# Kernel optimization log

Hardware: AMD Instinct MI355X
Metric: run time of the kernel (lower is better)

The kernel has to match this reference:

```python
import jax, jax.numpy as jnp
import numpy as np
from jax import lax

# SLAYER neuron / simulation constants (from netParams)
THETA = 10.0       # spike threshold
TAU_SR = 10.0      # synaptic (PSP) time constant
TAU_REF = 1.0      # refractory time constant
SCALE_REF = 2.0    # refractory scale
TAU_RHO = 1.0      # surrogate-gradient width (unused in fwd)
K_PSP = 32         # truncation length of SRM alpha kernel
K_REF = 16         # truncation length of refractory kernel

_t = np.arange(K_PSP, dtype=np.float64)
PSP_KERN = jnp.asarray((_t / TAU_SR) * np.exp(1.0 - _t / TAU_SR), jnp.float32)  # [K_PSP]
_tr = np.arange(1, K_REF + 1, dtype=np.float64)
REF_KERN = jnp.asarray(-SCALE_REF * THETA * (_tr / TAU_REF) * np.exp(1.0 - _tr / TAU_REF), jnp.float32)  # [K_REF]


def psp(x):
    """Causal temporal FIR filter with SRM alpha kernel; x: [..., T]."""
    sh = x.shape
    T = sh[-1]
    flat = x.reshape(-1, 1, T)                       # [B*, 1, T]
    k = PSP_KERN[::-1][None, None, :]                # correlation kernel (reversed)
    y = lax.conv_general_dilated(flat, k, (1,), [(K_PSP - 1, 0)])
    return y.reshape(sh)


def spike(u):
    """Threshold with refractory feedback, sequential over time. u: [..., T]."""
    uT = jnp.moveaxis(u, -1, 0)                      # [T, ...]
    buf0 = jnp.zeros(u.shape[:-1] + (K_REF,), u.dtype)

    def step(buf, ut):
        v = ut + buf[..., 0]
        s = (v >= THETA).astype(u.dtype)
        buf = jnp.concatenate([buf[..., 1:], jnp.zeros_like(buf[..., :1])], -1)
        buf = buf + s[..., None] * REF_KERN
        return buf, s

    _, sT = lax.scan(step, buf0, uT)
    return jnp.moveaxis(sT, 0, -1)


def conv_t(x, w, stride, pad):
    """2D conv applied independently per timestep. x: [N,C,H,W,T], w: [Co,C,kh,kw]."""
    N, C, H, W, T = x.shape
    xt = jnp.moveaxis(x, -1, 1).reshape(N * T, C, H, W)
    y = lax.conv_general_dilated(xt, w, (stride, stride), [(pad, pad), (pad, pad)])
    Co, Ho, Wo = y.shape[1], y.shape[2], y.shape[3]
    return jnp.moveaxis(y.reshape(N, T, Co, Ho, Wo), 1, -1)


def pool_t(x):
    """SLAYER sum-pool 2x2/s2 with weight 1.1*theta/kernel_area. x: [N,C,H,W,T]."""
    s = lax.reduce_window(x, np.float32(0.0), lax.add, (1, 1, 2, 2, 1), (1, 1, 2, 2, 1), 'VALID')
    return s * np.float32(1.1 * THETA / 4.0)


def setup_inputs() -> dict:
    key = jax.random.key(0)
    ks = jax.random.split(key, 5)
    spikeInput = (jax.random.uniform(ks[0], (4, 2, 256, 256, 50)) < 0.02).astype(jnp.float32)
    w1 = jax.random.normal(ks[1], (8, 2, 5, 5), jnp.float32) * 2.0
    w2 = jax.random.normal(ks[2], (16, 8, 3, 3), jnp.float32) * 1.5
    w3 = jax.random.normal(ks[3], (32, 16, 3, 3), jnp.float32) * 1.5
    w_fc = jax.random.normal(ks[4], (2, 32, 8, 8), jnp.float32) * 0.3
    return {"spikeInput": spikeInput, "w1": w1, "w2": w2, "w3": w3, "w_fc": w_fc}


def reference(spikeInput, w1, w2, w3, w_fc):
    x = spike(conv_t(psp(spikeInput), w1, 2, 1))   # [4,8,127,127,50]
    x = spike(pool_t(psp(x)))                      # [4,8,63,63,50]
    x = spike(conv_t(psp(x), w2, 2, 1))            # [4,16,32,32,50]
    x = spike(pool_t(psp(x)))                      # [4,16,16,16,50]
    x = spike(conv_t(psp(x), w3, 2, 1))            # [4,32,8,8,50]
    u = psp(x)
    out = jnp.einsum('ochw,nchwt->not', w_fc, u)   # dense over (C,H,W)
    return spike(out[:, :, None, None, :])         # [4,2,1,1,50]
```

## Files before the change

kernel.cpp:

```cpp
#include <hip/hip_runtime.h>
#include <cmath>

struct K32 { float k[32]; };
struct K16 { float k[16]; };

#define THETA 10.0f

__global__ __launch_bounds__(256)
void psp_kernel(const float* __restrict__ in, float* __restrict__ out,
                int nrows, K32 pk) {
  __shared__ __align__(16) float lds[128 * 50];
  const int rowBase = blockIdx.x * 128;
  const int tid = threadIdx.x;
  const int vr = min(128, nrows - rowBase);
  const int n4 = (vr * 50) >> 2;
  const float4* g4 = (const float4*)(in + (size_t)rowBase * 50);
  for (int i = tid; i < n4; i += 256) *(float4*)(&lds[4 * i]) = g4[i];
  __syncthreads();
  const int r = tid & 127;
  const int part = tid >> 7;
  const bool act = r < vr;
  float x[50];
  if (act) {
    if (part == 0) {
#pragma unroll
      for (int t = 0; t < 25; ++t) x[t] = lds[r * 50 + t];
    } else {
#pragma unroll
      for (int t = 0; t < 50; ++t) x[t] = lds[r * 50 + t];
    }
  }
  __syncthreads();
  if (act) {
    if (part == 0) {
#pragma unroll
      for (int t = 0; t < 25; ++t) {
        float a = 0.f;
#pragma unroll
        for (int k = 31; k >= 0; --k)
          if (t - k >= 0) a += x[t - k] * pk.k[k];
        lds[r * 50 + t] = a;
      }
    } else {
#pragma unroll
      for (int t = 25; t < 50; ++t) {
        float a = 0.f;
#pragma unroll
        for (int k = 31; k >= 0; --k)
          if (t - k >= 0) a += x[t - k] * pk.k[k];
        lds[r * 50 + t] = a;
      }
    }
  }
  __syncthreads();
  float4* o4 = (float4*)(out + (size_t)rowBase * 50);
  for (int i = tid; i < n4; i += 256) o4[i] = *(const float4*)(&lds[4 * i]);
}

template <int CIN, int COUT, int KK, int WT>
__global__ __launch_bounds__(256)
void conv_spike_kernel(const float* __restrict__ x, const float* __restrict__ w,
                       float* __restrict__ s, int N, int Hin, int Win,
                       int Hout, int Wout, K16 rk) {
  constexpr int XR = 2 * (WT - 1) + KK;
  constexpr int TW = 4 * WT;
  __shared__ float lds[COUT * TW * 51];
  const int tid = threadIdx.x;
  const int wave = tid >> 6;
  const int lane = tid & 63;
  const int groups = (Wout + TW - 1) / TW;
  const int group = blockIdx.x % groups;
  const int rest = blockIdx.x / groups;
  const int ho = rest % Hout;
  const int n = rest / Hout;
  const int wo0 = group * TW + wave * WT;
  const int tt = lane < 50 ? lane : 49;

  float acc[COUT][WT] = {};
  for (int c = 0; c < CIN; ++c) {
#pragma unroll
    for (int kh = 0; kh < KK; ++kh) {
      const int hi = 2 * ho + kh - 1;
      if ((unsigned)hi >= (unsigned)Hin) continue;
      float xr[XR];
#pragma unroll
      for (int i = 0; i < XR; ++i) {
        const int wi = 2 * wo0 - 1 + i;
        xr[i] = ((unsigned)wi < (unsigned)Win)
                    ? x[(((size_t)(n * CIN + c) * Hin + hi) * Win + wi) * 50 + tt]
                    : 0.f;
      }
#pragma unroll
      for (int co = 0; co < COUT; ++co)
#pragma unroll
        for (int kw = 0; kw < KK; ++kw) {
          const float wv = w[((co * CIN + c) * KK + kh) * KK + kw];
#pragma unroll
          for (int wl = 0; wl < WT; ++wl)
            acc[co][wl] += xr[2 * wl + kw] * wv;
        }
    }
  }

  if (lane < 50) {
#pragma unroll
    for (int co = 0; co < COUT; ++co)
#pragma unroll
      for (int wl = 0; wl < WT; ++wl)
        lds[(co * TW + wave * WT + wl) * 51 + lane] = acc[co][wl];
  }
  __syncthreads();
  if (tid < COUT * TW) {
    const int wol = tid % TW;
    if (group * TW + wol < Wout) {
      float buf[16];
#pragma unroll
      for (int j = 0; j < 16; ++j) buf[j] = 0.f;
#pragma unroll
      for (int t = 0; t < 50; ++t) {
        float v = lds[tid * 51 + t] + buf[t & 15];
        buf[t & 15] = 0.f;
        float sp = 0.f;
        if (v >= THETA) {
          sp = 1.f;
#pragma unroll
          for (int j = 0; j < 16; ++j) buf[(t + 1 + j) & 15] += rk.k[j];
        }
        lds[tid * 51 + t] = sp;
      }
    }
  }
  __syncthreads();
  const int nv = min(TW, Wout - group * TW);
  if (nv == TW) {
    constexpr int PER2 = TW * 25;
    for (int i2 = tid; i2 < COUT * PER2; i2 += 256) {
      const int co = i2 / PER2;
      const int r2 = i2 - co * PER2;
      const int wol = r2 / 25;
      const int j = r2 - wol * 25;
      float2 v;
      v.x = lds[(co * TW + wol) * 51 + 2 * j];
      v.y = lds[(co * TW + wol) * 51 + 2 * j + 1];
      *(float2*)(s + (((size_t)(n * COUT + co) * Hout + ho) * Wout + group * TW) * 50 + 2 * r2) = v;
    }
  } else {
    const int per = nv * 50;
    for (int i = tid; i < COUT * per; i += 256) {
      const int co = i / per;
      const int j = i - co * per;
      const int wol = j / 50;
      const int t = j - wol * 50;
      s[(((size_t)(n * COUT + co) * Hout + ho) * Wout + group * TW) * 50 + j] =
          lds[(co * TW + wol) * 51 + t];
    }
  }
}

__global__ __launch_bounds__(256)
void pps_kernel(const float* __restrict__ in, float* __restrict__ out,
                int Hin, int Win, int Hout, int Wout, int nseg,
                K32 pk, K16 rk) {
  __shared__ __align__(16) float lds[160 * 50];
  const int tid = threadIdx.x;
  const int seg = blockIdx.x % nseg;
  const int rest = blockIdx.x / nseg;
  const int ho = rest % Hout;
  const int nc = rest / Hout;
  const int wbase = seg * 64;
  const int nw = min(64, 2 * Wout - wbase);
  const int nwo = nw >> 1;
  const int span = nw * 50;
  const float* b0 = in + ((size_t)(nc * Hin + 2 * ho) * Win + wbase) * 50;
  const float* b1 = b0 + (size_t)Win * 50;
  const int n2 = span >> 1;
  for (int i = tid; i < n2; i += 256) {
    *(float2*)(&lds[2 * i]) = *(const float2*)(b0 + 2 * i);
    *(float2*)(&lds[span + 2 * i]) = *(const float2*)(b1 + 2 * i);
  }
  __syncthreads();
  const int r = tid & 127;
  const int part = tid >> 7;
  const bool act = r < 2 * nw;
  float x[50];
  if (act) {
    if (part == 0) {
#pragma unroll
      for (int t = 0; t < 25; ++t) x[t] = lds[r * 50 + t];
    } else {
#pragma unroll
      for (int t = 0; t < 50; ++t) x[t] = lds[r * 50 + t];
    }
  }
  __syncthreads();
  if (act) {
    if (part == 0) {
#pragma unroll
      for (int t = 0; t < 25; ++t) {
        float a = 0.f;
#pragma unroll
        for (int k = 31; k >= 0; --k)
          if (t - k >= 0) a += x[t - k] * pk.k[k];
        lds[r * 50 + t] = a;
      }
    } else {
#pragma unroll
      for (int t = 25; t < 50; ++t) {
        float a = 0.f;
#pragma unroll
        for (int k = 31; k >= 0; --k)
          if (t - k >= 0) a += x[t - k] * pk.k[k];
        lds[r * 50 + t] = a;
      }
    }
  }
  __syncthreads();
  if (tid < nwo) {
    float buf[16];
#pragma unroll
    for (int j = 0; j < 16; ++j) buf[j] = 0.f;
    const int r00 = (2 * tid) * 50, r01 = (2 * tid + 1) * 50;
    const int r10 = (nw + 2 * tid) * 50, r11 = (nw + 2 * tid + 1) * 50;
    const int ro = (2 * nw + tid) * 50;
#pragma unroll
    for (int t = 0; t < 50; ++t) {
      const float u0 = (((lds[r00 + t] + lds[r01 + t]) + lds[r10 + t]) + lds[r11 + t]) * 2.75f;
      float v = u0 + buf[t & 15];
      buf[t & 15] = 0.f;
      float sp = 0.f;
      if (v >= THETA) {
        sp = 1.f;
#pragma unroll
        for (int j = 0; j < 16; ++j) buf[(t + 1 + j) & 15] += rk.k[j];
      }
      lds[ro + t] = sp;
    }
  }
  __syncthreads();
  float* ob = out + ((size_t)(nc * Hout + ho) * Wout + seg * 32) * 50;
  const int base = 2 * nw * 50;
  for (int i = tid; i < nwo * 25; i += 256)
    *(float2*)(ob + 2 * i) = *(const float2*)(&lds[base + 2 * i]);
}

__global__ __launch_bounds__(512)
void fc_spike_kernel(const float* __restrict__ w, const float* __restrict__ u,
                     float* __restrict__ out, K16 rk) {
  __shared__ float lds[8 * 51];
  const int tid = threadIdx.x;
  const int wave = tid >> 6, lane = tid & 63;
  const int o = wave & 1, n = wave >> 1;
  const int tt = lane < 50 ? lane : 49;
  const float* wrow = w + (size_t)o * 2048;
  const float* ub = u + (size_t)n * 2048 * 50;
  float acc = 0.f;
#pragma unroll 32
  for (int i = 0; i < 2048; ++i) acc += wrow[i] * ub[(size_t)i * 50 + tt];
  if (lane < 50) lds[wave * 51 + lane] = acc;
  __syncthreads();
  if (tid < 8) {
    float buf[16];
#pragma unroll
    for (int j = 0; j < 16; ++j) buf[j] = 0.f;
#pragma unroll
    for (int t = 0; t < 50; ++t) {
      float v = lds[tid * 51 + t] + buf[t & 15];
      buf[t & 15] = 0.f;
      float sp = 0.f;
      if (v >= THETA) {
        sp = 1.f;
#pragma unroll
        for (int j = 0; j < 16; ++j) buf[(t + 1 + j) & 15] += rk.k[j];
      }
      out[tid * 50 + t] = sp;
    }
  }
}

extern "C" void kernel_launch(void* const* d_in, const int* in_sizes, int n_in,
                              void* d_out, int out_size, void* d_ws, size_t ws_size,
                              hipStream_t stream) {
  const float* xin = (const float*)d_in[0];
  const float* w1  = (const float*)d_in[1];
  const float* w2  = (const float*)d_in[2];
  const float* w3  = (const float*)d_in[3];
  const float* wfc = (const float*)d_in[4];
  float* out = (float*)d_out;

  float* R0 = (float*)d_ws;
  float* R1 = R0 + 26214400;

  K32 pk;
  for (int k = 0; k < 32; ++k)
    pk.k[k] = (float)(((double)k / 10.0) * exp(1.0 - (double)k / 10.0));
  K16 rk;
  for (int j = 0; j < 16; ++j) {
    const double tr = (double)(j + 1);
    rk.k[j] = (float)(-2.0 * 10.0 * tr * exp(1.0 - tr));
  }

  psp_kernel<<<4096, 256, 0, stream>>>(xin, R0, 524288, pk);
  conv_spike_kernel<2, 8, 5, 4><<<4 * 127 * 8, 256, 0, stream>>>(R0, w1, R1, 4, 256, 256, 127, 127, rk);
  pps_kernel<<<4 * 8 * 63 * 2, 256, 0, stream>>>(R1, R0, 127, 127, 63, 63, 2, pk, rk);
  psp_kernel<<<993, 256, 0, stream>>>(R0, R1, 127008, pk);
  conv_spike_kernel<8, 16, 3, 2><<<4 * 32 * 4, 256, 0, stream>>>(R1, w2, R0, 4, 63, 63, 32, 32, rk);
  pps_kernel<<<4 * 16 * 16, 256, 0, stream>>>(R0, R1, 32, 32, 16, 16, 1, pk, rk);
  psp_kernel<<<128, 256, 0, stream>>>(R1, R0, 16384, pk);
  conv_spike_kernel<16, 32, 3, 1><<<4 * 8 * 2, 256, 0, stream>>>(R0, w3, R1, 4, 16, 16, 8, 8, rk);
  psp_kernel<<<64, 256, 0, stream>>>(R1, R0, 8192, pk);
  fc_spike_kernel<<<1, 512, 0, stream>>>(wfc, R0, out, rk);
}
```

Measured before the change: 546.1 us.

## Fuse PSP filter into spike epilogues of pool and conv kernels

The pool-spike kernel now keeps its spike train in registers and applies the 32-tap PSP filter before writing out. The last conv-spike kernel can do the same through a template flag. This removes three standalone psp_kernel launches and their global read/write round-trips. Conv shapes also become template constants so index arithmetic folds at compile time. In exchange, the epilogue threads hold 50-element arrays, which raises register pressure, and the serial filter runs on fewer threads per block.

```diff
diff --git a/kernel.cpp b/kernel.cpp
--- a/kernel.cpp
+++ b/kernel.cpp
@@ -57,22 +57,22 @@
   for (int i = tid; i < n4; i += 256) o4[i] = *(const float4*)(&lds[4 * i]);
 }
 
-template <int CIN, int COUT, int KK, int WT>
+template <int CIN, int COUT, int KK, int WT, int HIN, int WIN, int HOUT, int WOUT,
+          bool PSP_OUT>
 __global__ __launch_bounds__(256)
 void conv_spike_kernel(const float* __restrict__ x, const float* __restrict__ w,
-                       float* __restrict__ s, int N, int Hin, int Win,
-                       int Hout, int Wout, K16 rk) {
+                       float* __restrict__ s, K32 pk, K16 rk) {
   constexpr int XR = 2 * (WT - 1) + KK;
   constexpr int TW = 4 * WT;
+  constexpr int GROUPS = (WOUT + TW - 1) / TW;
   __shared__ float lds[COUT * TW * 51];
   const int tid = threadIdx.x;
   const int wave = tid >> 6;
   const int lane = tid & 63;
-  const int groups = (Wout + TW - 1) / TW;
-  const int group = blockIdx.x % groups;
-  const int rest = blockIdx.x / groups;
-  const int ho = rest % Hout;
-  const int n = rest / Hout;
+  const int group = blockIdx.x % GROUPS;
+  const int rest = blockIdx.x / GROUPS;
+  const int ho = rest % HOUT;
+  const int n = rest / HOUT;
   const int wo0 = group * TW + wave * WT;
   const int tt = lane < 50 ? lane : 49;
 
@@ -81,13 +81,13 @@
 #pragma unroll
     for (int kh = 0; kh < KK; ++kh) {
       const int hi = 2 * ho + kh - 1;
-      if ((unsigned)hi >= (unsigned)Hin) continue;
+      if ((unsigned)hi >= (unsigned)HIN) continue;
       float xr[XR];
 #pragma unroll
       for (int i = 0; i < XR; ++i) {
         const int wi = 2 * wo0 - 1 + i;
-        xr[i] = ((unsigned)wi < (unsigned)Win)
-                    ? x[(((size_t)(n * CIN + c) * Hin + hi) * Win + wi) * 50 + tt]
+        xr[i] = ((unsigned)wi < (unsigned)WIN)
+                    ? x[(((size_t)(n * CIN + c) * HIN + hi) * WIN + wi) * 50 + tt]
                     : 0.f;
       }
 #pragma unroll
@@ -112,8 +112,9 @@
   __syncthreads();
   if (tid < COUT * TW) {
     const int wol = tid % TW;
-    if (group * TW + wol < Wout) {
+    if (group * TW + wol < WOUT) {
       float buf[16];
+      float y[PSP_OUT ? 50 : 1];
 #pragma unroll
       for (int j = 0; j < 16; ++j) buf[j] = 0.f;
 #pragma unroll
@@ -126,12 +127,22 @@
 #pragma unroll
           for (int j = 0; j < 16; ++j) buf[(t + 1 + j) & 15] += rk.k[j];
         }
-        lds[tid * 51 + t] = sp;
-      }
-    }
-  }
-  __syncthreads();
-  const int nv = min(TW, Wout - group * TW);
+        if (PSP_OUT) y[t] = sp; else lds[tid * 51 + t] = sp;
+      }
+      if (PSP_OUT) {
+#pragma unroll
+        for (int t = 0; t < 50; ++t) {
+          float a = 0.f;
+#pragma unroll
+          for (int k = 31; k >= 0; --k)
+            if (t - k >= 0) a += y[t - k] * pk.k[k];
+          lds[tid * 51 + t] = a;
+        }
+      }
+    }
+  }
+  __syncthreads();
+  const int nv = min(TW, WOUT - group * TW);
   if (nv == TW) {
     constexpr int PER2 = TW * 25;
     for (int i2 = tid; i2 < COUT * PER2; i2 += 256) {
@@ -142,7 +153,7 @@
       float2 v;
       v.x = lds[(co * TW + wol) * 51 + 2 * j];
       v.y = lds[(co * TW + wol) * 51 + 2 * j + 1];
-      *(float2*)(s + (((size_t)(n * COUT + co) * Hout + ho) * Wout + group * TW) * 50 + 2 * r2) = v;
+      *(float2*)(s + (((size_t)(n * COUT + co) * HOUT + ho) * WOUT + group * TW) * 50 + 2 * r2) = v;
     }
   } else {
     const int per = nv * 50;
@@ -151,7 +162,7 @@
       const int j = i - co * per;
       const int wol = j / 50;
       const int t = j - wol * 50;
-      s[(((size_t)(n * COUT + co) * Hout + ho) * Wout + group * TW) * 50 + j] =
+      s[(((size_t)(n * COUT + co) * HOUT + ho) * WOUT + group * TW) * 50 + j] =
           lds[(co * TW + wol) * 51 + t];
     }
   }
@@ -217,6 +228,7 @@
   __syncthreads();
   if (tid < nwo) {
     float buf[16];
+    float sp[50];
 #pragma unroll
     for (int j = 0; j < 16; ++j) buf[j] = 0.f;
     const int r00 = (2 * tid) * 50, r01 = (2 * tid + 1) * 50;
@@ -227,13 +239,21 @@
       const float u0 = (((lds[r00 + t] + lds[r01 + t]) + lds[r10 + t]) + lds[r11 + t]) * 2.75f;
       float v = u0 + buf[t & 15];
       buf[t & 15] = 0.f;
-      float sp = 0.f;
+      float spv = 0.f;
       if (v >= THETA) {
-        sp = 1.f;
+        spv = 1.f;
 #pragma unroll
         for (int j = 0; j < 16; ++j) buf[(t + 1 + j) & 15] += rk.k[j];
       }
-      lds[ro + t] = sp;
+      sp[t] = spv;
+    }
+#pragma unroll
+    for (int t = 0; t < 50; ++t) {
+      float a = 0.f;
+#pragma unroll
+      for (int k = 31; k >= 0; --k)
+        if (t - k >= 0) a += sp[t - k] * pk.k[k];
+      lds[ro + t] = a;
     }
   }
   __syncthreads();
@@ -300,13 +320,13 @@
   }
 
   psp_kernel<<<4096, 256, 0, stream>>>(xin, R0, 524288, pk);
-  conv_spike_kernel<2, 8, 5, 4><<<4 * 127 * 8, 256, 0, stream>>>(R0, w1, R1, 4, 256, 256, 127, 127, rk);
+  conv_spike_kernel<2, 8, 5, 4, 256, 256, 127, 127, false>
+      <<<4 * 127 * 8, 256, 0, stream>>>(R0, w1, R1, pk, rk);
   pps_kernel<<<4 * 8 * 63 * 2, 256, 0, stream>>>(R1, R0, 127, 127, 63, 63, 2, pk, rk);
-  psp_kernel<<<993, 256, 0, stream>>>(R0, R1, 127008, pk);
-  conv_spike_kernel<8, 16, 3, 2><<<4 * 32 * 4, 256, 0, stream>>>(R1, w2, R0, 4, 63, 63, 32, 32, rk);
-  pps_kernel<<<4 * 16 * 16, 256, 0, stream>>>(R0, R1, 32, 32, 16, 16, 1, pk, rk);
-  psp_kernel<<<128, 256, 0, stream>>>(R1, R0, 16384, pk);
-  conv_spike_kernel<16, 32, 3, 1><<<4 * 8 * 2, 256, 0, stream>>>(R0, w3, R1, 4, 16, 16, 8, 8, rk);
-  psp_kernel<<<64, 256, 0, stream>>>(R1, R0, 8192, pk);
-  fc_spike_kernel<<<1, 512, 0, stream>>>(wfc, R0, out, rk);
-}
+  conv_spike_kernel<8, 16, 3, 2, 63, 63, 32, 32, false>
+      <<<4 * 32 * 4, 256, 0, stream>>>(R0, w2, R1, pk, rk);
+  pps_kernel<<<4 * 16 * 16, 256, 0, stream>>>(R1, R0, 32, 32, 16, 16, 1, pk, rk);
+  conv_spike_kernel<16, 32, 3, 1, 16, 16, 8, 8, true>
+      <<<4 * 8 * 2, 256, 0, stream>>>(R0, w3, R1, pk, rk);
+  fc_spike_kernel<<<1, 512, 0, stream>>>(wfc, R1, out, rk);
+}
```

After: 642.5 us. 1.18x slower.
